# Performance work log

Measured on AMD Instinct MI355X. Metric: run time of the kernel, lower is better.

Reference implementation:

```python
import math
import jax, jax.numpy as jnp
import numpy as np

NUM_EXPERTS = 64
HIDDEN = 2048
BATCH, SEQ = 8, 2048


def setup_inputs() -> dict:
    key = jax.random.key(0)
    k1, k2 = jax.random.split(key)
    hidden_states = jax.random.normal(k1, (BATCH, SEQ, HIDDEN), dtype=jnp.float32)
    classifier_weight = jax.random.normal(k2, (HIDDEN, NUM_EXPERTS), dtype=jnp.float32) * (1.0 / math.sqrt(HIDDEN))
    return {"hidden_states": hidden_states, "classifier_weight": classifier_weight}


def _route_tokens(router_logits):
    # router_logits: (tokens, experts). second_expert_policy='all',
    # normalize_router_prob_before_dropping=False, batch_prioritized_routing=True,
    # training mode -> capacity = 2*ceil(tokens/experts), no padding mask.
    n_tokens, n_experts = router_logits.shape
    router_probs = jax.nn.softmax(router_logits, axis=-1)  # router_dtype=float32

    top_1_idx = jnp.argmax(router_probs, axis=-1)
    top_1_mask = jax.nn.one_hot(top_1_idx, n_experts, dtype=router_probs.dtype)
    logits_except_top_1 = jnp.where(top_1_mask > 0, -jnp.inf, router_logits)
    top_2_idx = jnp.argmax(logits_except_top_1, axis=-1)
    top_2_mask = jax.nn.one_hot(top_2_idx, n_experts, dtype=router_probs.dtype)

    # batch-prioritized routing: sort tokens by -max prob, cumsum positions per expert
    importance = -jnp.max(router_probs, axis=-1)  # (tokens,)
    order = jnp.argsort(importance)
    inv_order = jnp.argsort(order)
    sorted_1 = top_1_mask[order]
    locations1 = ((jnp.cumsum(sorted_1, axis=0) - 1.0) * sorted_1)[inv_order]
    sorted_2 = top_2_mask[order]
    locations2 = ((jnp.cumsum(sorted_2, axis=0) - 1.0) * sorted_2)[inv_order]
    locations2 = locations2 + jnp.sum(top_1_mask, axis=0, keepdims=True)

    expert_capacity = 2 * math.ceil(n_tokens / n_experts)  # training path, expert_capacity=None
    top_1_mask = top_1_mask * (locations1 < expert_capacity).astype(top_1_mask.dtype)
    top_2_mask = top_2_mask * (locations2 < expert_capacity).astype(top_2_mask.dtype)

    # normalize AFTER dropping (normalize_router_prob_before_dropping=False)
    top_1_max_probs = jnp.sum(router_probs * top_1_mask, axis=-1)
    top_2_max_probs = jnp.sum(router_probs * top_2_mask, axis=-1)
    denom = jnp.clip(top_1_max_probs + top_2_max_probs, jnp.finfo(router_probs.dtype).eps, None)
    gates1 = (top_1_max_probs / denom)[:, None] * top_1_mask
    gates2 = (top_2_max_probs / denom)[:, None] * top_2_mask
    return top_1_mask, gates1 + gates2


def reference(hidden_states, classifier_weight):
    b, s, h = hidden_states.shape
    x = hidden_states.reshape(b * s, h)
    router_logits = x @ classifier_weight  # (tokens, experts), bias=False
    top_1_mask, router_probs = _route_tokens(router_logits)
    return top_1_mask, router_probs
```

## Files before the change

### kernel.cpp

```cpp
#include <hip/hip_runtime.h>
#include <math.h>

#define TOKENS      16384
#define HID         2048
#define EXPERTS     64
#define CAPSLOT     1024
#define CAP         512
#define KSPLIT      4
#define KCH         512

__device__ __forceinline__ void fma8(float* a, float s, float4 w0, float4 w1) {
    a[0] = fmaf(s, w0.x, a[0]); a[1] = fmaf(s, w0.y, a[1]);
    a[2] = fmaf(s, w0.z, a[2]); a[3] = fmaf(s, w0.w, a[3]);
    a[4] = fmaf(s, w1.x, a[4]); a[5] = fmaf(s, w1.y, a[5]);
    a[6] = fmaf(s, w1.z, a[6]); a[7] = fmaf(s, w1.w, a[7]);
}

__global__ __launch_bounds__(256, 1) void k_partial(
    const float* __restrict__ x, const float* __restrict__ W,
    float* __restrict__ partial)
{
    __shared__ float wl[KCH * EXPERTS];

    const int tid = threadIdx.x;
    const int tb = blockIdx.x & 63;
    const int kc = blockIdx.x >> 6;
    const int k0 = kc * KCH;

    {
        const float4* src = (const float4*)(W + (size_t)k0 * EXPERTS);
        float4* dst = (float4*)wl;
        #pragma unroll
        for (int i = 0; i < (KCH * EXPERTS / 4) / 256; ++i)
            dst[i * 256 + tid] = src[i * 256 + tid];
    }
    __syncthreads();

    const int lane = tid & 63;
    const int wv   = tid >> 6;
    const int tg   = lane >> 3;
    const int eg   = lane & 7;
    const int tok0 = tb * 256 + wv * 64 + tg * 8;
    const float* xb = x + (size_t)tok0 * HID + k0;

    float acc[8][8];
    #pragma unroll
    for (int i = 0; i < 8; ++i)
        #pragma unroll
        for (int e = 0; e < 8; ++e) acc[i][e] = 0.f;

    float4 xv[8];
    #pragma unroll
    for (int i = 0; i < 8; ++i)
        xv[i] = *(const float4*)(xb + (size_t)i * HID);

    #pragma unroll 2
    for (int k4 = 0; k4 < KCH; k4 += 4) {
        float4 xn[8];
        const bool more = (k4 + 4 < KCH);
        if (more) {
            #pragma unroll
            for (int i = 0; i < 8; ++i)
                xn[i] = *(const float4*)(xb + (size_t)i * HID + k4 + 4);
        }

        float4 w0[4], w1[4];
        #pragma unroll
        for (int kk = 0; kk < 4; ++kk) {
            const float* wp = &wl[(k4 + kk) * EXPERTS + eg * 8];
            w0[kk] = *(const float4*)wp;
            w1[kk] = *(const float4*)(wp + 4);
        }

        #pragma unroll
        for (int i = 0; i < 8; ++i) {
            fma8(acc[i], xv[i].x, w0[0], w1[0]);
            fma8(acc[i], xv[i].y, w0[1], w1[1]);
            fma8(acc[i], xv[i].z, w0[2], w1[2]);
            fma8(acc[i], xv[i].w, w0[3], w1[3]);
        }

        if (more) {
            #pragma unroll
            for (int i = 0; i < 8; ++i) xv[i] = xn[i];
        }
    }

    float* pb = partial + ((size_t)kc * TOKENS + tok0) * EXPERTS + eg * 8;
    #pragma unroll
    for (int i = 0; i < 8; ++i) {
        *(float4*)(pb + (size_t)i * EXPERTS) =
            make_float4(acc[i][0], acc[i][1], acc[i][2], acc[i][3]);
        *(float4*)(pb + (size_t)i * EXPERTS + 4) =
            make_float4(acc[i][4], acc[i][5], acc[i][6], acc[i][7]);
    }
}

__global__ __launch_bounds__(256) void k_route(
    const float* __restrict__ partial,
    float* __restrict__ p1o, float* __restrict__ p2o,
    int* __restrict__ top1o, int* __restrict__ top2o)
{
    const int tid   = threadIdx.x;
    const int e     = tid & 63;
    const int token = blockIdx.x * 4 + (tid >> 6);

    float logit = 0.f;
    #pragma unroll
    for (int c = 0; c < KSPLIT; ++c)
        logit += partial[((size_t)c * TOKENS + token) * EXPERTS + e];

    float bv = logit; int be = e;
    #pragma unroll
    for (int m = 32; m >= 1; m >>= 1) {
        float ov = __shfl_xor(bv, m);
        int   oe = __shfl_xor(be, m);
        if (ov > bv || (ov == bv && oe < be)) { bv = ov; be = oe; }
    }
    const float m1 = bv;
    const int   e1 = be;

    float bv2 = (e == e1) ? -INFINITY : logit;
    int   be2 = (e == e1) ? (1 << 30) : e;
    #pragma unroll
    for (int m = 32; m >= 1; m >>= 1) {
        float ov = __shfl_xor(bv2, m);
        int   oe = __shfl_xor(be2, m);
        if (ov > bv2 || (ov == bv2 && oe < be2)) { bv2 = ov; be2 = oe; }
    }
    const int e2 = be2;

    float s = expf(logit - m1);
    #pragma unroll
    for (int m = 32; m >= 1; m >>= 1) s += __shfl_xor(s, m);

    if (e == 0) {
        p1o[token]   = 1.0f / s;
        p2o[token]   = expf(bv2 - m1) / s;
        top1o[token] = e1;
        top2o[token] = e2;
    }
}

__global__ __launch_bounds__(256) void k_rank(
    const float* __restrict__ p1,
    const int* __restrict__ top1, const int* __restrict__ top2,
    int* __restrict__ keep1, int* __restrict__ keep2)
{
    __shared__ float skey[CAPSLOT];
    __shared__ int   stok[CAPSLOT];
    __shared__ int   cnt;

    const int e   = blockIdx.x;
    const int tid = threadIdx.x;

    if (tid == 0) cnt = 0;
    __syncthreads();
    for (int t = tid; t < TOKENS; t += 256) {
        if (top1[t] == e) {
            int i = atomicAdd(&cnt, 1);
            if (i < CAPSLOT) { stok[i] = t; skey[i] = p1[t]; }
        }
    }
    __syncthreads();
    const int n1_raw = cnt;
    const int n1 = min(n1_raw, CAPSLOT);

    for (int i = tid; i < n1; i += 256) {
        const float ki = skey[i];
        const int   ti = stok[i];
        int r = 0;
        for (int j = 0; j < n1; ++j)
            r += (skey[j] > ki || (skey[j] == ki && stok[j] < ti)) ? 1 : 0;
        keep1[ti] = (r < CAP) ? 1 : 0;
    }
    __syncthreads();

    if (tid == 0) cnt = 0;
    __syncthreads();
    for (int t = tid; t < TOKENS; t += 256) {
        if (top2[t] == e) {
            int i = atomicAdd(&cnt, 1);
            if (i < CAPSLOT) { stok[i] = t; skey[i] = p1[t]; }
        }
    }
    __syncthreads();
    const int n2 = min(cnt, CAPSLOT);

    for (int i = tid; i < n2; i += 256) {
        const float ki = skey[i];
        const int   ti = stok[i];
        int r = n1_raw;
        for (int j = 0; j < n2; ++j)
            r += (skey[j] > ki || (skey[j] == ki && stok[j] < ti)) ? 1 : 0;
        keep2[ti] = (r < CAP) ? 1 : 0;
    }
}

__global__ __launch_bounds__(256) void k_out(
    const float* __restrict__ p1, const float* __restrict__ p2,
    const int* __restrict__ top1, const int* __restrict__ top2,
    const int* __restrict__ keep1, const int* __restrict__ keep2,
    float* __restrict__ out)
{
    const int tid   = threadIdx.x;
    const int token = blockIdx.x * 16 + (tid >> 4);
    const int eb    = (tid & 15) * 4;

    const int  k1 = keep1[token];
    const int  k2 = keep2[token];
    const float P1 = k1 ? p1[token] : 0.0f;
    const float P2 = k2 ? p2[token] : 0.0f;
    const float denom = fmaxf(P1 + P2, 1.1920929e-07f);
    const float g1 = P1 / denom;
    const float g2 = P2 / denom;
    const int e1 = top1[token];
    const int e2 = top2[token];

    float4 mv, pv;
    mv.x = (k1 && e1 == eb + 0) ? 1.0f : 0.0f;
    mv.y = (k1 && e1 == eb + 1) ? 1.0f : 0.0f;
    mv.z = (k1 && e1 == eb + 2) ? 1.0f : 0.0f;
    mv.w = (k1 && e1 == eb + 3) ? 1.0f : 0.0f;
    pv.x = (k1 && e1 == eb + 0) ? g1 : ((k2 && e2 == eb + 0) ? g2 : 0.0f);
    pv.y = (k1 && e1 == eb + 1) ? g1 : ((k2 && e2 == eb + 1) ? g2 : 0.0f);
    pv.z = (k1 && e1 == eb + 2) ? g1 : ((k2 && e2 == eb + 2) ? g2 : 0.0f);
    pv.w = (k1 && e1 == eb + 3) ? g1 : ((k2 && e2 == eb + 3) ? g2 : 0.0f);

    *(float4*)(out + (size_t)token * EXPERTS + eb) = mv;
    *(float4*)(out + (size_t)TOKENS * EXPERTS + (size_t)token * EXPERTS + eb) = pv;
}

extern "C" void kernel_launch(void* const* d_in, const int* in_sizes, int n_in,
                              void* d_out, int out_size, void* d_ws, size_t ws_size,
                              hipStream_t stream)
{
    const float* x = (const float*)d_in[0];
    const float* W = (const float*)d_in[1];
    float* out = (float*)d_out;

    char* ws = (char*)d_ws;
    float* partial = (float*)ws;
    float* p1    = partial + (size_t)KSPLIT * TOKENS * EXPERTS;
    float* p2    = p1 + TOKENS;
    int*   top1  = (int*)(p2 + TOKENS);
    int*   top2  = top1 + TOKENS;
    int*   keep1 = top2 + TOKENS;
    int*   keep2 = keep1 + TOKENS;

    k_partial<<<64 * KSPLIT, 256, 0, stream>>>(x, W, partial);
    k_route<<<TOKENS / 4, 256, 0, stream>>>(partial, p1, p2, top1, top2);
    k_rank<<<EXPERTS, 256, 0, stream>>>(p1, top1, top2, keep1, keep2);
    k_out<<<TOKENS / 16, 256, 0, stream>>>(
        p1, p2, top1, top2, keep1, keep2, out);
}
```

Measured before the change: 301.8 us.

## Fuse router GEMM and top-2 routing with in-block split-K reduction

Replaces the split-K GEMM that wrote partial logits to global memory, and the separate routing kernel that re-read them, with one kernel. Each 512-thread block handles 32 tokens, with its 8 waves each covering a 256-wide K slice, and reduces the partials through shared memory in a tree. Wave 0 then computes the top-1 and top-2 experts and the softmax terms directly from registers. This removes the partial-logit round trip (about 16 MB written and read back) and one launch. In exchange, W is now read from global memory or cache instead of being staged in LDS, and each thread keeps a smaller 4x8 register tile.

```diff
diff --git a/kernel.cpp b/kernel.cpp
--- a/kernel.cpp
+++ b/kernel.cpp
@@ -6,8 +6,6 @@
 #define EXPERTS     64
 #define CAPSLOT     1024
 #define CAP         512
-#define KSPLIT      4
-#define KCH         512
 
 __device__ __forceinline__ void fma8(float* a, float s, float4 w0, float4 w1) {
     a[0] = fmaf(s, w0.x, a[0]); a[1] = fmaf(s, w0.y, a[1]);
@@ -16,129 +14,124 @@
     a[6] = fmaf(s, w1.z, a[6]); a[7] = fmaf(s, w1.w, a[7]);
 }
 
-__global__ __launch_bounds__(256, 1) void k_partial(
+__global__ __launch_bounds__(512, 4) void k_gemm_route(
     const float* __restrict__ x, const float* __restrict__ W,
-    float* __restrict__ partial)
-{
-    __shared__ float wl[KCH * EXPERTS];
-
-    const int tid = threadIdx.x;
-    const int tb = blockIdx.x & 63;
-    const int kc = blockIdx.x >> 6;
-    const int k0 = kc * KCH;
-
-    {
-        const float4* src = (const float4*)(W + (size_t)k0 * EXPERTS);
-        float4* dst = (float4*)wl;
-        #pragma unroll
-        for (int i = 0; i < (KCH * EXPERTS / 4) / 256; ++i)
-            dst[i * 256 + tid] = src[i * 256 + tid];
-    }
-    __syncthreads();
-
+    float* __restrict__ p1o, float* __restrict__ p2o,
+    int* __restrict__ top1o, int* __restrict__ top2o)
+{
+    __shared__ float red[4 * 2048];
+
+    const int tid  = threadIdx.x;
+    const int w    = tid >> 6;
     const int lane = tid & 63;
-    const int wv   = tid >> 6;
     const int tg   = lane >> 3;
     const int eg   = lane & 7;
-    const int tok0 = tb * 256 + wv * 64 + tg * 8;
-    const float* xb = x + (size_t)tok0 * HID + k0;
-
-    float acc[8][8];
+    const int tok0 = blockIdx.x * 32;
+
+    const float* xb = x + (size_t)(tok0 + tg * 4) * HID + w * 256;
+    const float* wb = W + (size_t)(w * 256) * EXPERTS + eg * 8;
+
+    float acc[4][8];
     #pragma unroll
-    for (int i = 0; i < 8; ++i)
-        #pragma unroll
-        for (int e = 0; e < 8; ++e) acc[i][e] = 0.f;
-
-    float4 xv[8];
-    #pragma unroll
-    for (int i = 0; i < 8; ++i)
-        xv[i] = *(const float4*)(xb + (size_t)i * HID);
-
-    #pragma unroll 2
-    for (int k4 = 0; k4 < KCH; k4 += 4) {
-        float4 xn[8];
-        const bool more = (k4 + 4 < KCH);
-        if (more) {
-            #pragma unroll
-            for (int i = 0; i < 8; ++i)
-                xn[i] = *(const float4*)(xb + (size_t)i * HID + k4 + 4);
-        }
+    for (int i = 0; i < 4; ++i)
+        #pragma unroll
+        for (int j = 0; j < 8; ++j) acc[i][j] = 0.f;
+
+    for (int k4 = 0; k4 < 256; k4 += 4) {
+        float4 xv[4];
+        #pragma unroll
+        for (int i = 0; i < 4; ++i)
+            xv[i] = *(const float4*)(xb + (size_t)i * HID + k4);
 
         float4 w0[4], w1[4];
         #pragma unroll
         for (int kk = 0; kk < 4; ++kk) {
-            const float* wp = &wl[(k4 + kk) * EXPERTS + eg * 8];
+            const float* wp = wb + (size_t)(k4 + kk) * EXPERTS;
             w0[kk] = *(const float4*)wp;
             w1[kk] = *(const float4*)(wp + 4);
         }
 
         #pragma unroll
-        for (int i = 0; i < 8; ++i) {
+        for (int i = 0; i < 4; ++i) {
             fma8(acc[i], xv[i].x, w0[0], w1[0]);
             fma8(acc[i], xv[i].y, w0[1], w1[1]);
             fma8(acc[i], xv[i].z, w0[2], w1[2]);
             fma8(acc[i], xv[i].w, w0[3], w1[3]);
         }
-
-        if (more) {
-            #pragma unroll
-            for (int i = 0; i < 8; ++i) xv[i] = xn[i];
-        }
-    }
-
-    float* pb = partial + ((size_t)kc * TOKENS + tok0) * EXPERTS + eg * 8;
-    #pragma unroll
-    for (int i = 0; i < 8; ++i) {
-        *(float4*)(pb + (size_t)i * EXPERTS) =
-            make_float4(acc[i][0], acc[i][1], acc[i][2], acc[i][3]);
-        *(float4*)(pb + (size_t)i * EXPERTS + 4) =
-            make_float4(acc[i][4], acc[i][5], acc[i][6], acc[i][7]);
-    }
-}
-
-__global__ __launch_bounds__(256) void k_route(
-    const float* __restrict__ partial,
-    float* __restrict__ p1o, float* __restrict__ p2o,
-    int* __restrict__ top1o, int* __restrict__ top2o)
-{
-    const int tid   = threadIdx.x;
-    const int e     = tid & 63;
-    const int token = blockIdx.x * 4 + (tid >> 6);
-
-    float logit = 0.f;
-    #pragma unroll
-    for (int c = 0; c < KSPLIT; ++c)
-        logit += partial[((size_t)c * TOKENS + token) * EXPERTS + e];
-
-    float bv = logit; int be = e;
-    #pragma unroll
-    for (int m = 32; m >= 1; m >>= 1) {
-        float ov = __shfl_xor(bv, m);
-        int   oe = __shfl_xor(be, m);
-        if (ov > bv || (ov == bv && oe < be)) { bv = ov; be = oe; }
-    }
-    const float m1 = bv;
-    const int   e1 = be;
-
-    float bv2 = (e == e1) ? -INFINITY : logit;
-    int   be2 = (e == e1) ? (1 << 30) : e;
-    #pragma unroll
-    for (int m = 32; m >= 1; m >>= 1) {
-        float ov = __shfl_xor(bv2, m);
-        int   oe = __shfl_xor(be2, m);
-        if (ov > bv2 || (ov == bv2 && oe < be2)) { bv2 = ov; be2 = oe; }
-    }
-    const int e2 = be2;
-
-    float s = expf(logit - m1);
-    #pragma unroll
-    for (int m = 32; m >= 1; m >>= 1) s += __shfl_xor(s, m);
-
-    if (e == 0) {
-        p1o[token]   = 1.0f / s;
-        p2o[token]   = expf(bv2 - m1) / s;
-        top1o[token] = e1;
-        top2o[token] = e2;
+    }
+
+    auto WR = [&](int slot) {
+        float* b = red + slot * 2048 + lane * 4;
+        #pragma unroll
+        for (int q = 0; q < 8; ++q) {
+            const int i = q >> 1, j0 = (q & 1) * 4;
+            *(float4*)(b + q * 256) = make_float4(
+                acc[i][j0 + 0], acc[i][j0 + 1], acc[i][j0 + 2], acc[i][j0 + 3]);
+        }
+    };
+    auto AD = [&](int slot) {
+        const float* b = red + slot * 2048 + lane * 4;
+        #pragma unroll
+        for (int q = 0; q < 8; ++q) {
+            const int i = q >> 1, j0 = (q & 1) * 4;
+            float4 r = *(const float4*)(b + q * 256);
+            acc[i][j0 + 0] += r.x; acc[i][j0 + 1] += r.y;
+            acc[i][j0 + 2] += r.z; acc[i][j0 + 3] += r.w;
+        }
+    };
+
+    if (w >= 4) WR(w - 4);
+    __syncthreads();
+    if (w < 4) { AD(w); if (w >= 2) WR(w); }
+    __syncthreads();
+    if (w < 2) { AD(w + 2); if (w == 1) WR(1); }
+    __syncthreads();
+
+    if (w == 0) {
+        AD(1);
+
+        #pragma unroll
+        for (int i = 0; i < 4; ++i) {
+            float bv = acc[i][0]; int be = eg * 8;
+            #pragma unroll
+            for (int j = 1; j < 8; ++j)
+                if (acc[i][j] > bv) { bv = acc[i][j]; be = eg * 8 + j; }
+            #pragma unroll
+            for (int m = 1; m <= 4; m <<= 1) {
+                float ov = __shfl_xor(bv, m);
+                int   oe = __shfl_xor(be, m);
+                if (ov > bv || (ov == bv && oe < be)) { bv = ov; be = oe; }
+            }
+            const float m1 = bv;
+            const int   e1 = be;
+
+            float bv2 = -INFINITY; int be2 = 1 << 30;
+            #pragma unroll
+            for (int j = 0; j < 8; ++j) {
+                const int e = eg * 8 + j;
+                if (e != e1 && acc[i][j] > bv2) { bv2 = acc[i][j]; be2 = e; }
+            }
+            #pragma unroll
+            for (int m = 1; m <= 4; m <<= 1) {
+                float ov = __shfl_xor(bv2, m);
+                int   oe = __shfl_xor(be2, m);
+                if (ov > bv2 || (ov == bv2 && oe < be2)) { bv2 = ov; be2 = oe; }
+            }
+
+            float s = 0.f;
+            #pragma unroll
+            for (int j = 0; j < 8; ++j) s += expf(acc[i][j] - m1);
+            #pragma unroll
+            for (int m = 1; m <= 4; m <<= 1) s += __shfl_xor(s, m);
+
+            if (eg == 0) {
+                const int t = tok0 + tg * 4 + i;
+                p1o[t]   = 1.0f / s;
+                p2o[t]   = expf(bv2 - m1) / s;
+                top1o[t] = e1;
+                top2o[t] = be2;
+            }
+        }
     }
 }
 
@@ -239,17 +232,14 @@
     const float* W = (const float*)d_in[1];
     float* out = (float*)d_out;
 
-    char* ws = (char*)d_ws;
-    float* partial = (float*)ws;
-    float* p1    = partial + (size_t)KSPLIT * TOKENS * EXPERTS;
+    float* p1    = (float*)d_ws;
     float* p2    = p1 + TOKENS;
     int*   top1  = (int*)(p2 + TOKENS);
     int*   top2  = top1 + TOKENS;
     int*   keep1 = top2 + TOKENS;
     int*   keep2 = keep1 + TOKENS;
 
-    k_partial<<<64 * KSPLIT, 256, 0, stream>>>(x, W, partial);
-    k_route<<<TOKENS / 4, 256, 0, stream>>>(partial, p1, p2, top1, top2);
+    k_gemm_route<<<512, 512, 0, stream>>>(x, W, p1, p2, top1, top2);
     k_rank<<<EXPERTS, 256, 0, stream>>>(p1, top1, top2, keep1, keep2);
     k_out<<<TOKENS / 16, 256, 0, stream>>>(
         p1, p2, top1, top2, keep1, keep2, out);
```

New measurement: 346.9 us. +14.9%, slower.

## Bucket tokens per expert during routing and deepen K-split of router GEMM

Applied to the files above, without the earlier changes.

The routing kernel now atomically appends each token's top-1 and top-2 expert choice and key into per-expert buckets. The rank kernel no longer scans all tokens twice per expert, and runs 128 blocks (one per expert and choice) instead of 64. The GEMM split goes from 4 to 8 K-chunks when the workspace is large enough, giving 512 blocks with half the shared memory each and a relaxed launch bound for more occupancy. This costs global atomics, more partial-sum traffic to reduce, and a counter reset done inside the first GEMM block.

```diff
diff --git a/kernel.cpp b/kernel.cpp
--- a/kernel.cpp
+++ b/kernel.cpp
@@ -6,8 +6,6 @@
 #define EXPERTS     64
 #define CAPSLOT     1024
 #define CAP         512
-#define KSPLIT      4
-#define KCH         512
 
 __device__ __forceinline__ void fma8(float* a, float s, float4 w0, float4 w1) {
     a[0] = fmaf(s, w0.x, a[0]); a[1] = fmaf(s, w0.y, a[1]);
@@ -16,9 +14,10 @@
     a[6] = fmaf(s, w1.z, a[6]); a[7] = fmaf(s, w1.w, a[7]);
 }
 
-__global__ __launch_bounds__(256, 1) void k_partial(
+template<int KCH>
+__global__ __launch_bounds__(256) void k_partial(
     const float* __restrict__ x, const float* __restrict__ W,
-    float* __restrict__ partial)
+    float* __restrict__ partial, int* __restrict__ cnts)
 {
     __shared__ float wl[KCH * EXPERTS];
 
@@ -26,6 +25,10 @@
     const int tb = blockIdx.x & 63;
     const int kc = blockIdx.x >> 6;
     const int k0 = kc * KCH;
+
+    if (blockIdx.x == 0) {
+        for (int i = tid; i < 128 * 16; i += 256) cnts[i] = 0;
+    }
 
     {
         const float4* src = (const float4*)(W + (size_t)k0 * EXPERTS);
@@ -96,10 +99,12 @@
     }
 }
 
+template<int KSPLIT>
 __global__ __launch_bounds__(256) void k_route(
     const float* __restrict__ partial,
     float* __restrict__ p1o, float* __restrict__ p2o,
-    int* __restrict__ top1o, int* __restrict__ top2o)
+    int* __restrict__ top1o, int* __restrict__ top2o,
+    int* __restrict__ cnts, float* __restrict__ bkey, int* __restrict__ btok)
 {
     const int tid   = threadIdx.x;
     const int e     = tid & 63;
@@ -135,65 +140,56 @@
     for (int m = 32; m >= 1; m >>= 1) s += __shfl_xor(s, m);
 
     if (e == 0) {
-        p1o[token]   = 1.0f / s;
+        const float P1 = 1.0f / s;
+        p1o[token]   = P1;
         p2o[token]   = expf(bv2 - m1) / s;
         top1o[token] = e1;
         top2o[token] = e2;
+
+        int s1 = atomicAdd(&cnts[e1 * 16], 1);
+        if (s1 < CAPSLOT) {
+            bkey[(size_t)e1 * CAPSLOT + s1] = P1;
+            btok[(size_t)e1 * CAPSLOT + s1] = token;
+        }
+        int s2 = atomicAdd(&cnts[(64 + e2) * 16], 1);
+        if (s2 < CAPSLOT) {
+            bkey[(size_t)(64 + e2) * CAPSLOT + s2] = P1;
+            btok[(size_t)(64 + e2) * CAPSLOT + s2] = token;
+        }
     }
 }
 
 __global__ __launch_bounds__(256) void k_rank(
-    const float* __restrict__ p1,
-    const int* __restrict__ top1, const int* __restrict__ top2,
+    const int* __restrict__ cnts,
+    const float* __restrict__ bkey, const int* __restrict__ btok,
     int* __restrict__ keep1, int* __restrict__ keep2)
 {
     __shared__ float skey[CAPSLOT];
     __shared__ int   stok[CAPSLOT];
-    __shared__ int   cnt;
-
-    const int e   = blockIdx.x;
-    const int tid = threadIdx.x;
-
-    if (tid == 0) cnt = 0;
+
+    const int b    = blockIdx.x;
+    const int mode = b >> 6;
+    const int e    = b & 63;
+    const int tid  = threadIdx.x;
+
+    const int n_raw = cnts[b * 16];
+    const int n     = min(n_raw, CAPSLOT);
+    const int base  = mode ? cnts[e * 16] : 0;
+
+    for (int i = tid; i < n; i += 256) {
+        skey[i] = bkey[(size_t)b * CAPSLOT + i];
+        stok[i] = btok[(size_t)b * CAPSLOT + i];
+    }
     __syncthreads();
-    for (int t = tid; t < TOKENS; t += 256) {
-        if (top1[t] == e) {
-            int i = atomicAdd(&cnt, 1);
-            if (i < CAPSLOT) { stok[i] = t; skey[i] = p1[t]; }
-        }
-    }
-    __syncthreads();
-    const int n1_raw = cnt;
-    const int n1 = min(n1_raw, CAPSLOT);
-
-    for (int i = tid; i < n1; i += 256) {
+
+    int* __restrict__ keep = mode ? keep2 : keep1;
+    for (int i = tid; i < n; i += 256) {
         const float ki = skey[i];
         const int   ti = stok[i];
-        int r = 0;
-        for (int j = 0; j < n1; ++j)
+        int r = base;
+        for (int j = 0; j < n; ++j)
             r += (skey[j] > ki || (skey[j] == ki && stok[j] < ti)) ? 1 : 0;
-        keep1[ti] = (r < CAP) ? 1 : 0;
-    }
-    __syncthreads();
-
-    if (tid == 0) cnt = 0;
-    __syncthreads();
-    for (int t = tid; t < TOKENS; t += 256) {
-        if (top2[t] == e) {
-            int i = atomicAdd(&cnt, 1);
-            if (i < CAPSLOT) { stok[i] = t; skey[i] = p1[t]; }
-        }
-    }
-    __syncthreads();
-    const int n2 = min(cnt, CAPSLOT);
-
-    for (int i = tid; i < n2; i += 256) {
-        const float ki = skey[i];
-        const int   ti = stok[i];
-        int r = n1_raw;
-        for (int j = 0; j < n2; ++j)
-            r += (skey[j] > ki || (skey[j] == ki && stok[j] < ti)) ? 1 : 0;
-        keep2[ti] = (r < CAP) ? 1 : 0;
+        keep[ti] = (r < CAP) ? 1 : 0;
     }
 }
 
@@ -239,18 +235,34 @@
     const float* W = (const float*)d_in[1];
     float* out = (float*)d_out;
 
-    char* ws = (char*)d_ws;
-    float* partial = (float*)ws;
-    float* p1    = partial + (size_t)KSPLIT * TOKENS * EXPERTS;
+    const size_t extras_f = 6 * (size_t)TOKENS
+                          + 128 * 16
+                          + 2 * 128 * (size_t)CAPSLOT;
+    const size_t need8 = ((size_t)8 * TOKENS * EXPERTS + extras_f) * 4;
+    const bool big = (ws_size == 0) || (ws_size >= need8);
+    const int  ks  = big ? 8 : 4;
+
+    float* partial = (float*)d_ws;
+    float* p1    = partial + (size_t)ks * TOKENS * EXPERTS;
     float* p2    = p1 + TOKENS;
     int*   top1  = (int*)(p2 + TOKENS);
     int*   top2  = top1 + TOKENS;
     int*   keep1 = top2 + TOKENS;
     int*   keep2 = keep1 + TOKENS;
-
-    k_partial<<<64 * KSPLIT, 256, 0, stream>>>(x, W, partial);
-    k_route<<<TOKENS / 4, 256, 0, stream>>>(partial, p1, p2, top1, top2);
-    k_rank<<<EXPERTS, 256, 0, stream>>>(p1, top1, top2, keep1, keep2);
+    int*   cnts  = keep2 + TOKENS;
+    float* bkey  = (float*)(cnts + 128 * 16);
+    int*   btok  = (int*)(bkey + 128 * CAPSLOT);
+
+    if (big) {
+        k_partial<256><<<64 * 8, 256, 0, stream>>>(x, W, partial, cnts);
+        k_route<8><<<TOKENS / 4, 256, 0, stream>>>(
+            partial, p1, p2, top1, top2, cnts, bkey, btok);
+    } else {
+        k_partial<512><<<64 * 4, 256, 0, stream>>>(x, W, partial, cnts);
+        k_route<4><<<TOKENS / 4, 256, 0, stream>>>(
+            partial, p1, p2, top1, top2, cnts, bkey, btok);
+    }
+    k_rank<<<2 * EXPERTS, 256, 0, stream>>>(cnts, bkey, btok, keep1, keep2);
     k_out<<<TOKENS / 16, 256, 0, stream>>>(
         p1, p2, top1, top2, keep1, keep2, out);
 }
```

Result: faster. 258.4 us (-14.4%).
